# Optimization experiments

Hardware: AMD Instinct MI355X
Metric: run time of the kernel (lower is better)

The kernel has to match this reference:

```python
import jax, jax.numpy as jnp
import numpy as np

V = 16384      # total nodes
G = 32         # nodes per graph (512 graphs)
D = 256        # node embedding dim == hidden_size
N = 8          # heads
H = 32         # head size
I = 1024       # intermediate size
LN_EPS = 1e-12


def _layer_norm(x, g, b):
    mu = jnp.mean(x, axis=-1, keepdims=True)
    var = jnp.mean(jnp.square(x - mu), axis=-1, keepdims=True)
    return (x - mu) * jax.lax.rsqrt(var + LN_EPS) * g + b


def setup_inputs() -> dict:
    key = jax.random.key(0)
    ks = jax.random.split(key, 5)
    node_embeddings = jax.random.normal(ks[0], (V, D), jnp.float32)
    # fully-connected pairs within each graph of size G (sorted by source node)
    idx = np.arange(V, dtype=np.int32).reshape(-1, G)          # [num_graphs, G]
    src = np.repeat(idx, G, axis=1).reshape(-1)                # [P]
    dst = np.tile(idx, (1, G)).reshape(-1)                     # [P]
    in_graph_node_pairs = jnp.asarray(np.stack([src, dst], axis=-1))  # [P, 2]
    s = 0.02
    return {
        "node_embeddings": node_embeddings,
        "in_graph_node_pairs": in_graph_node_pairs,
        "W_qkv": jax.random.normal(ks[1], (D, 3 * N * H), jnp.float32) * s,
        "W_o": jax.random.normal(ks[2], (N * H, D), jnp.float32) * s,
        "ln1_g": jnp.ones((D,), jnp.float32),
        "ln1_b": jnp.zeros((D,), jnp.float32),
        "W_i": jax.random.normal(ks[3], (D, I), jnp.float32) * s,
        "W_out2": jax.random.normal(ks[4], (I, D), jnp.float32) * s,
        "ln2_g": jnp.ones((D,), jnp.float32),
        "ln2_b": jnp.zeros((D,), jnp.float32),
    }


def reference(node_embeddings, in_graph_node_pairs, W_qkv, W_o, ln1_g, ln1_b,
              W_i, W_out2, ln2_g, ln2_b):
    nV = node_embeddings.shape[0]
    src = in_graph_node_pairs[:, 0]
    dst = in_graph_node_pairs[:, 1]
    # QKV projection -> [V, N, 3H] -> split
    qkv = (node_embeddings @ W_qkv).reshape(nV, N, 3 * H)
    q, k, v = jnp.split(qkv, 3, axis=-1)                       # each [V, N, H]
    # per-pair scores [P, N]
    scores = jnp.einsum('phi,phi->ph', q[src], k[dst]) / jnp.sqrt(jnp.float32(H))
    # segment softmax over source node, all heads at once
    m = jax.ops.segment_max(scores, src, num_segments=nV)       # [V, N]
    e = jnp.exp(scores - m[src])
    denom = jax.ops.segment_sum(e, src, num_segments=nV)        # [V, N]
    w = e / denom[src]                                          # [P, N]
    # weighted value scatter-sum -> [V, N, H]
    wv = w[:, :, None] * v[dst]
    att = jax.ops.segment_sum(wv, src, num_segments=nV).reshape(nV, N * H)
    # output projection + residual + LN
    pre = _layer_norm(att @ W_o + node_embeddings, ln1_g, ln1_b)
    inter = jax.nn.gelu(pre @ W_i, approximate=False)
    out = _layer_norm(inter @ W_out2 + pre, ln2_g, ln2_b)
    return out
```

## Files before the change

kernel.cpp:

```cpp
#include <hip/hip_runtime.h>
#include <math.h>

#define V 16384
#define D 256
#define NH 256
#define THREE_NH 768
#define IDIM 1024
#define LN_EPS 1e-12f

typedef short s16x8 __attribute__((ext_vector_type(8)));
typedef float f32x4 __attribute__((ext_vector_type(4)));

__device__ inline unsigned short f2bf(float f) {
    unsigned u = __float_as_uint(f);
    u += 0x7fffu + ((u >> 16) & 1u);
    return (unsigned short)(u >> 16);
}
__device__ inline float bf2f(unsigned short s) {
    return __uint_as_float(((unsigned)s) << 16);
}
__device__ inline float bflo(unsigned v) { return __uint_as_float(v << 16); }
__device__ inline float bfhi(unsigned v) { return __uint_as_float(v & 0xffff0000u); }

__device__ inline void gl2lds16(const unsigned short* g, unsigned short* l) {
    __builtin_amdgcn_global_load_lds(
        (__attribute__((address_space(1))) void*)(g),
        (__attribute__((address_space(3))) void*)(l), 16, 0, 0);
}

template <int ROWS_T>
__device__ inline void stage(const unsigned short* __restrict__ src, size_t row0,
                             int ldk, int k0, unsigned short* lds, int wv, int lane) {
    constexpr int PER_WAVE = ROWS_T / 32;
    #pragma unroll
    for (int i = 0; i < PER_WAVE; ++i) {
        const int seg = wv * PER_WAVE + i;
        const int r = seg * 8 + (lane >> 3);
        const int c = (lane & 7) ^ (r & 7);
        gl2lds16(src + (row0 + (size_t)r) * ldk + k0 + c * 8, lds + seg * 512);
    }
}

__device__ inline s16x8 fragld(const unsigned short* lds, int row, int chunk) {
    return *(const s16x8*)&lds[row * 64 + ((chunk ^ (row & 7)) << 3)];
}

__global__ __launch_bounds__(256) void prep(const float* __restrict__ X,
                                            unsigned short* __restrict__ Xb,
                                            const float* __restrict__ Wqkv,
                                            const float* __restrict__ Wo,
                                            const float* __restrict__ Wi,
                                            const float* __restrict__ Wo2,
                                            unsigned short* __restrict__ WqkvT,
                                            unsigned short* __restrict__ WoT,
                                            unsigned short* __restrict__ WiT,
                                            unsigned short* __restrict__ Wo2T) {
    const int b = blockIdx.x, t = threadIdx.x;
    if (b >= 768) {
        int i = (b - 768) * 256 + t;
        float4 v = ((const float4*)X)[i];
        ushort4 o;
        o.x = f2bf(v.x); o.y = f2bf(v.y); o.z = f2bf(v.z); o.w = f2bf(v.w);
        ((ushort4*)Xb)[i] = o;
        return;
    }
    __shared__ float tile[32][33];
    const float* W; unsigned short* Wt; int K, N, bx, by;
    if (b < 192)      { W = Wqkv; Wt = WqkvT; K = 256;  N = 768;  bx = b & 7;          by = b >> 3; }
    else if (b < 256) { W = Wo;   Wt = WoT;   K = 256;  N = 256;  bx = (b - 192) & 7;  by = (b - 192) >> 3; }
    else if (b < 512) { W = Wi;   Wt = WiT;   K = 256;  N = 1024; bx = (b - 256) & 7;  by = (b - 256) >> 3; }
    else              { W = Wo2;  Wt = Wo2T;  K = 1024; N = 256;  bx = (b - 512) & 31; by = (b - 512) >> 5; }
    const int k0 = bx * 32, n0 = by * 32;
    #pragma unroll
    for (int p = 0; p < 4; ++p) {
        int idx = t + p * 256, r = idx >> 5, c = idx & 31;
        tile[r][c] = W[(size_t)(k0 + r) * N + n0 + c];
    }
    __syncthreads();
    #pragma unroll
    for (int p = 0; p < 4; ++p) {
        int idx = t + p * 256, r = idx >> 5, c = idx & 31;
        Wt[(size_t)(n0 + r) * K + k0 + c] = f2bf(tile[c][r]);
    }
}

template <int K, int N, int EPI>
__global__ __launch_bounds__(256) void gemm128(const unsigned short* __restrict__ A,
                                               const unsigned short* __restrict__ Bt,
                                               unsigned short* __restrict__ C) {
    __shared__ unsigned short As[128 * 64];
    __shared__ unsigned short Bs[128 * 64];
    const int t = threadIdx.x;
    const int r0 = blockIdx.x * 128, c0 = blockIdx.y * 128;
    const int wv = t >> 6, lane = t & 63, q = lane >> 4, l16 = lane & 15;
    const int wr = (wv >> 1) * 64, wc = (wv & 1) * 64;
    f32x4 acc[4][4] = {};

    for (int k0 = 0; k0 < K; k0 += 64) {
        __syncthreads();
        stage<128>(A,  (size_t)r0, K, k0, As, wv, lane);
        stage<128>(Bt, (size_t)c0, K, k0, Bs, wv, lane);
        __builtin_amdgcn_s_waitcnt(0);
        __syncthreads();
        #pragma unroll
        for (int kk2 = 0; kk2 < 2; ++kk2) {
            s16x8 af[4], bfr[4];
            #pragma unroll
            for (int mf = 0; mf < 4; ++mf)
                af[mf] = fragld(As, wr + mf * 16 + l16, kk2 * 4 + q);
            #pragma unroll
            for (int nf = 0; nf < 4; ++nf)
                bfr[nf] = fragld(Bs, wc + nf * 16 + l16, kk2 * 4 + q);
            #pragma unroll
            for (int mf = 0; mf < 4; ++mf)
                #pragma unroll
                for (int nf = 0; nf < 4; ++nf)
                    acc[mf][nf] = __builtin_amdgcn_mfma_f32_16x16x32_bf16(af[mf], bfr[nf], acc[mf][nf], 0, 0, 0);
        }
    }

    #pragma unroll
    for (int mf = 0; mf < 4; ++mf)
        #pragma unroll
        for (int nf = 0; nf < 4; ++nf) {
            const int cg = c0 + wc + nf * 16 + l16;
            #pragma unroll
            for (int r = 0; r < 4; ++r) {
                const int rg = r0 + wr + mf * 16 + q * 4 + r;
                float v = acc[mf][nf][r];
                if (EPI == 1) v = 0.5f * v * (1.f + erff(v * 0.70710678118654752f));
                C[(size_t)rg * N + cg] = f2bf(v);
            }
        }
}

template <int K, bool OUTF, bool RESBF>
__global__ __launch_bounds__(256) void gemm_ln(const unsigned short* __restrict__ A,
                                               const unsigned short* __restrict__ Bt,
                                               const void* __restrict__ resv,
                                               const float* __restrict__ gamma,
                                               const float* __restrict__ beta,
                                               float* __restrict__ outf,
                                               unsigned short* __restrict__ outb) {
    __shared__ unsigned short As[32 * 64];
    __shared__ unsigned short Bs[256 * 64];
    __shared__ float2 partial[4][32];
    __shared__ float2 stats[32];
    const int t = threadIdx.x, r0 = blockIdx.x * 32;
    const int wv = t >> 6, lane = t & 63, q = lane >> 4, l16 = lane & 15;
    const int wc = wv * 64;
    f32x4 acc[2][4] = {};

    for (int k0 = 0; k0 < K; k0 += 64) {
        __syncthreads();
        stage<32>(A, (size_t)r0, K, k0, As, wv, lane);
        stage<256>(Bt, 0, K, k0, Bs, wv, lane);
        __builtin_amdgcn_s_waitcnt(0);
        __syncthreads();
        #pragma unroll
        for (int kk2 = 0; kk2 < 2; ++kk2) {
            s16x8 af[2], bfr[4];
            #pragma unroll
            for (int mf = 0; mf < 2; ++mf)
                af[mf] = fragld(As, mf * 16 + l16, kk2 * 4 + q);
            #pragma unroll
            for (int nf = 0; nf < 4; ++nf)
                bfr[nf] = fragld(Bs, wc + nf * 16 + l16, kk2 * 4 + q);
            #pragma unroll
            for (int mf = 0; mf < 2; ++mf)
                #pragma unroll
                for (int nf = 0; nf < 4; ++nf)
                    acc[mf][nf] = __builtin_amdgcn_mfma_f32_16x16x32_bf16(af[mf], bfr[nf], acc[mf][nf], 0, 0, 0);
        }
    }

    #pragma unroll
    for (int mf = 0; mf < 2; ++mf)
        #pragma unroll
        for (int nf = 0; nf < 4; ++nf) {
            const int cg = wc + nf * 16 + l16;
            #pragma unroll
            for (int r = 0; r < 4; ++r) {
                const size_t idx = (size_t)(r0 + mf * 16 + q * 4 + r) * NH + cg;
                float rv;
                if (RESBF) rv = bf2f(((const unsigned short*)resv)[idx]);
                else       rv = ((const float*)resv)[idx];
                acc[mf][nf][r] += rv;
            }
        }

    #pragma unroll
    for (int mf = 0; mf < 2; ++mf) {
        float s[4] = {0.f, 0.f, 0.f, 0.f}, ss[4] = {0.f, 0.f, 0.f, 0.f};
        #pragma unroll
        for (int nf = 0; nf < 4; ++nf)
            #pragma unroll
            for (int r = 0; r < 4; ++r) {
                float v = acc[mf][nf][r];
                s[r] += v; ss[r] += v * v;
            }
        #pragma unroll
        for (int off = 1; off < 16; off <<= 1)
            #pragma unroll
            for (int r = 0; r < 4; ++r) {
                s[r]  += __shfl_xor(s[r],  off);
                ss[r] += __shfl_xor(ss[r], off);
            }
        if (l16 == 0)
            #pragma unroll
            for (int r = 0; r < 4; ++r)
                partial[wv][mf * 16 + q * 4 + r] = make_float2(s[r], ss[r]);
    }
    __syncthreads();
    if (t < 32) {
        float s = 0.f, ss = 0.f;
        #pragma unroll
        for (int w = 0; w < 4; ++w) { s += partial[w][t].x; ss += partial[w][t].y; }
        float mu  = s * (1.f / 256.f);
        float var = ss * (1.f / 256.f) - mu * mu;
        stats[t] = make_float2(mu, rsqrtf(var + LN_EPS));
    }
    __syncthreads();

    #pragma unroll
    for (int mf = 0; mf < 2; ++mf)
        #pragma unroll
        for (int nf = 0; nf < 4; ++nf) {
            const int cg = wc + nf * 16 + l16;
            const float g = gamma[cg], b = beta[cg];
            #pragma unroll
            for (int r = 0; r < 4; ++r) {
                const int rl = mf * 16 + q * 4 + r;
                const float2 st = stats[rl];
                float v = (acc[mf][nf][r] - st.x) * st.y * g + b;
                const size_t idx = (size_t)(r0 + rl) * NH + cg;
                if (OUTF) outf[idx] = v;
                else      outb[idx] = f2bf(v);
            }
        }
}

#define LDR 776
__global__ __launch_bounds__(256) void attln(const unsigned short* __restrict__ qkv,
                                             const unsigned short* __restrict__ WoT,
                                             const float* __restrict__ X,
                                             const float* __restrict__ gamma,
                                             const float* __restrict__ beta,
                                             unsigned short* __restrict__ preb) {
    __shared__ unsigned short smem[33536 + 320];
    unsigned short* s  = smem;
    unsigned short* pt = smem + 24832;
    unsigned short* at = smem;
    unsigned short* Bs = smem + 8192;
    float2* partial = (float2*)(smem + 24832);
    float2* stats   = (float2*)(smem + 24832 + 512);

    const int g = blockIdx.x;
    const int t = threadIdx.x;
    const int h = t >> 5, u = t & 31;
    const int ub = u & 7;
    const int us = u >> 3;
    const int qc = h * 96;

    const unsigned short* src = qkv + (size_t)g * 32 * THREE_NH;
    #pragma unroll
    for (int pp = 0; pp < 12; ++pp) {
        int c = t + pp * 256;
        int row = c / 96, col8 = c % 96;
        s16x8 vv = *(const s16x8*)&src[c * 8];
        *(s16x8*)&s[row * LDR + col8 * 8] = vv;
    }
    __syncthreads();

    float sc[4][8];
    #pragma unroll
    for (int di = 0; di < 4; ++di)
        #pragma unroll
        for (int dj = 0; dj < 8; ++dj) sc[di][dj] = 0.f;

    for (int kq = 0; kq < 8; ++kq) {
        float qv[4][4];
        #pragma unroll
        for (int di = 0; di < 4; ++di) {
            uint2 v = *(const uint2*)&s[(ub + 8 * di) * LDR + qc + 4 * kq];
            qv[di][0] = bflo(v.x); qv[di][1] = bfhi(v.x);
            qv[di][2] = bflo(v.y); qv[di][3] = bfhi(v.y);
        }
        #pragma unroll
        for (int dj = 0; dj < 8; ++dj) {
            uint2 v = *(const uint2*)&s[(us + 4 * dj) * LDR + qc + 32 + 4 * kq];
            float kv[4];
            kv[0] = bflo(v.x); kv[1] = bfhi(v.x);
            kv[2] = bflo(v.y); kv[3] = bfhi(v.y);
            #pragma unroll
            for (int di = 0; di < 4; ++di)
                #pragma unroll
                for (int kk = 0; kk < 4; ++kk)
                    sc[di][dj] = fmaf(qv[di][kk], kv[kk], sc[di][dj]);
        }
    }

    #pragma unroll
    for (int di = 0; di < 4; ++di) {
        float m = sc[di][0];
        #pragma unroll
        for (int dj = 1; dj < 8; ++dj) m = fmaxf(m, sc[di][dj]);
        m = fmaxf(m, __shfl_xor(m, 8));
        m = fmaxf(m, __shfl_xor(m, 16));
        float sum = 0.f;
        #pragma unroll
        for (int dj = 0; dj < 8; ++dj) {
            float e = __expf((sc[di][dj] - m) * 0.17677669529663687f);
            sc[di][dj] = e;
            sum += e;
        }
        sum += __shfl_xor(sum, 8);
        sum += __shfl_xor(sum, 16);
        float inv = 1.f / sum;
        const int rb = h * 1088 + (ub + 8 * di) * 34;
        #pragma unroll
        for (int dj = 0; dj < 8; ++dj)
            pt[rb + us + 4 * dj] = f2bf(sc[di][dj] * inv);
    }
    __syncthreads();

    const int vc = qc + 64, d0 = us * 8;
    float o[4][8];
    #pragma unroll
    for (int di = 0; di < 4; ++di)
        #pragma unroll
        for (int dd = 0; dd < 8; ++dd) o[di][dd] = 0.f;

    for (int j = 0; j < 32; ++j) {
        float pv[4];
        #pragma unroll
        for (int di = 0; di < 4; ++di)
            pv[di] = bf2f(pt[h * 1088 + (ub + 8 * di) * 34 + j]);
        #pragma unroll
        for (int dq = 0; dq < 2; ++dq) {
            uint2 v = *(const uint2*)&s[j * LDR + vc + d0 + 4 * dq];
            float v0 = bflo(v.x), v1 = bfhi(v.x), v2 = bflo(v.y), v3 = bfhi(v.y);
            #pragma unroll
            for (int di = 0; di < 4; ++di) {
                o[di][dq * 4 + 0] = fmaf(pv[di], v0, o[di][dq * 4 + 0]);
                o[di][dq * 4 + 1] = fmaf(pv[di], v1, o[di][dq * 4 + 1]);
                o[di][dq * 4 + 2] = fmaf(pv[di], v2, o[di][dq * 4 + 2]);
                o[di][dq * 4 + 3] = fmaf(pv[di], v3, o[di][dq * 4 + 3]);
            }
        }
    }
    __syncthreads();

    {
        const int col = h * 32 + d0;
        const int kb = col >> 6, c = (col & 63) >> 3;
        #pragma unroll
        for (int di = 0; di < 4; ++di) {
            const int i = ub + 8 * di;
            s16x8 ov;
            #pragma unroll
            for (int dd = 0; dd < 8; ++dd) ov[dd] = (short)f2bf(o[di][dd]);
            *(s16x8*)&at[kb * 2048 + i * 64 + ((c ^ (i & 7)) << 3)] = ov;
        }
    }

    const int wv = t >> 6, lane = t & 63, q = lane >> 4, l16 = lane & 15;
    const int wc = wv * 64;
    const int r0 = g * 32;
    f32x4 acc[2][4] = {};

    for (int k0 = 0; k0 < 256; k0 += 64) {
        __syncthreads();
        stage<256>(WoT, 0, 256, k0, Bs, wv, lane);
        __builtin_amdgcn_s_waitcnt(0);
        __syncthreads();
        const unsigned short* atk = at + (k0 >> 6) * 2048;
        #pragma unroll
        for (int kk2 = 0; kk2 < 2; ++kk2) {
            s16x8 af[2], bfr[4];
            #pragma unroll
            for (int mf = 0; mf < 2; ++mf)
                af[mf] = fragld(atk, mf * 16 + l16, kk2 * 4 + q);
            #pragma unroll
            for (int nf = 0; nf < 4; ++nf)
                bfr[nf] = fragld(Bs, wc + nf * 16 + l16, kk2 * 4 + q);
            #pragma unroll
            for (int mf = 0; mf < 2; ++mf)
                #pragma unroll
                for (int nf = 0; nf < 4; ++nf)
                    acc[mf][nf] = __builtin_amdgcn_mfma_f32_16x16x32_bf16(af[mf], bfr[nf], acc[mf][nf], 0, 0, 0);
        }
    }

    #pragma unroll
    for (int mf = 0; mf < 2; ++mf)
        #pragma unroll
        for (int nf = 0; nf < 4; ++nf) {
            const int cg = wc + nf * 16 + l16;
            #pragma unroll
            for (int r = 0; r < 4; ++r)
                acc[mf][nf][r] += X[(size_t)(r0 + mf * 16 + q * 4 + r) * NH + cg];
        }

    #pragma unroll
    for (int mf = 0; mf < 2; ++mf) {
        float sp[4] = {0.f, 0.f, 0.f, 0.f}, ssp[4] = {0.f, 0.f, 0.f, 0.f};
        #pragma unroll
        for (int nf = 0; nf < 4; ++nf)
            #pragma unroll
            for (int r = 0; r < 4; ++r) {
                float v = acc[mf][nf][r];
                sp[r] += v; ssp[r] += v * v;
            }
        #pragma unroll
        for (int off = 1; off < 16; off <<= 1)
            #pragma unroll
            for (int r = 0; r < 4; ++r) {
                sp[r]  += __shfl_xor(sp[r],  off);
                ssp[r] += __shfl_xor(ssp[r], off);
            }
        if (l16 == 0)
            #pragma unroll
            for (int r = 0; r < 4; ++r)
                partial[wv * 32 + mf * 16 + q * 4 + r] = make_float2(sp[r], ssp[r]);
    }
    __syncthreads();
    if (t < 32) {
        float sv = 0.f, ssv = 0.f;
        #pragma unroll
        for (int w = 0; w < 4; ++w) { sv += partial[w * 32 + t].x; ssv += partial[w * 32 + t].y; }
        float mu  = sv * (1.f / 256.f);
        float var = ssv * (1.f / 256.f) - mu * mu;
        stats[t] = make_float2(mu, rsqrtf(var + LN_EPS));
    }
    __syncthreads();

    #pragma unroll
    for (int mf = 0; mf < 2; ++mf)
        #pragma unroll
        for (int nf = 0; nf < 4; ++nf) {
            const int cg = wc + nf * 16 + l16;
            const float gm = gamma[cg], bt = beta[cg];
            #pragma unroll
            for (int r = 0; r < 4; ++r) {
                const int rl = mf * 16 + q * 4 + r;
                const float2 st = stats[rl];
                float v = (acc[mf][nf][r] - st.x) * st.y * gm + bt;
                preb[(size_t)(r0 + rl) * NH + cg] = f2bf(v);
            }
        }
}

extern "C" void kernel_launch(void* const* d_in, const int* in_sizes, int n_in,
                              void* d_out, int out_size, void* d_ws, size_t ws_size,
                              hipStream_t stream) {
    const float* X      = (const float*)d_in[0];
    const float* W_qkv  = (const float*)d_in[2];
    const float* W_o    = (const float*)d_in[3];
    const float* ln1_g  = (const float*)d_in[4];
    const float* ln1_b  = (const float*)d_in[5];
    const float* W_i    = (const float*)d_in[6];
    const float* W_out2 = (const float*)d_in[7];
    const float* ln2_g  = (const float*)d_in[8];
    const float* ln2_b  = (const float*)d_in[9];
    float* out = (float*)d_out;

    char* ws = (char*)d_ws;
    unsigned short* Xbf   = (unsigned short*)(ws);
    unsigned short* qkvb  = (unsigned short*)(ws + 8388608);
    unsigned short* preb  = (unsigned short*)(ws + 58720256);
    unsigned short* WqkvT = (unsigned short*)(ws + 67108864);
    unsigned short* WoT   = (unsigned short*)(ws + 67502080);
    unsigned short* WiT   = (unsigned short*)(ws + 67633152);
    unsigned short* Wo2T  = (unsigned short*)(ws + 68157440);
    unsigned short* interb = (unsigned short*)(ws);

    dim3 blk(256);
    hipLaunchKernelGGL(prep, dim3(768 + V * D / 4 / 256), blk, 0, stream,
                       X, Xbf, W_qkv, W_o, W_i, W_out2, WqkvT, WoT, WiT, Wo2T);

    hipLaunchKernelGGL((gemm128<D, THREE_NH, 0>), dim3(V / 128, THREE_NH / 128), blk, 0, stream,
                       Xbf, WqkvT, qkvb);
    hipLaunchKernelGGL(attln, dim3(V / 32), blk, 0, stream,
                       qkvb, WoT, X, ln1_g, ln1_b, preb);
    hipLaunchKernelGGL((gemm128<D, IDIM, 1>), dim3(V / 128, IDIM / 128), blk, 0, stream,
                       preb, WiT, interb);
    hipLaunchKernelGGL((gemm_ln<IDIM, true, true>), dim3(V / 32), blk, 0, stream,
                       interb, Wo2T, (const void*)preb, ln2_g, ln2_b, out, (unsigned short*)nullptr);
}
```

Before: 164.8 us.

## Fuse all five kernels into one persistent kernel with grid barriers

```diff
diff --git a/kernel.cpp b/kernel.cpp
--- a/kernel.cpp
+++ b/kernel.cpp
@@ -45,53 +45,30 @@
     return *(const s16x8*)&lds[row * 64 + ((chunk ^ (row & 7)) << 3)];
 }
 
-__global__ __launch_bounds__(256) void prep(const float* __restrict__ X,
-                                            unsigned short* __restrict__ Xb,
-                                            const float* __restrict__ Wqkv,
-                                            const float* __restrict__ Wo,
-                                            const float* __restrict__ Wi,
-                                            const float* __restrict__ Wo2,
-                                            unsigned short* __restrict__ WqkvT,
-                                            unsigned short* __restrict__ WoT,
-                                            unsigned short* __restrict__ WiT,
-                                            unsigned short* __restrict__ Wo2T) {
-    const int b = blockIdx.x, t = threadIdx.x;
-    if (b >= 768) {
-        int i = (b - 768) * 256 + t;
-        float4 v = ((const float4*)X)[i];
-        ushort4 o;
-        o.x = f2bf(v.x); o.y = f2bf(v.y); o.z = f2bf(v.z); o.w = f2bf(v.w);
-        ((ushort4*)Xb)[i] = o;
-        return;
-    }
-    __shared__ float tile[32][33];
-    const float* W; unsigned short* Wt; int K, N, bx, by;
-    if (b < 192)      { W = Wqkv; Wt = WqkvT; K = 256;  N = 768;  bx = b & 7;          by = b >> 3; }
-    else if (b < 256) { W = Wo;   Wt = WoT;   K = 256;  N = 256;  bx = (b - 192) & 7;  by = (b - 192) >> 3; }
-    else if (b < 512) { W = Wi;   Wt = WiT;   K = 256;  N = 1024; bx = (b - 256) & 7;  by = (b - 256) >> 3; }
-    else              { W = Wo2;  Wt = Wo2T;  K = 1024; N = 256;  bx = (b - 512) & 31; by = (b - 512) >> 5; }
-    const int k0 = bx * 32, n0 = by * 32;
-    #pragma unroll
-    for (int p = 0; p < 4; ++p) {
-        int idx = t + p * 256, r = idx >> 5, c = idx & 31;
-        tile[r][c] = W[(size_t)(k0 + r) * N + n0 + c];
-    }
+__device__ inline void gridbar(unsigned* ctr) {
     __syncthreads();
-    #pragma unroll
-    for (int p = 0; p < 4; ++p) {
-        int idx = t + p * 256, r = idx >> 5, c = idx & 31;
-        Wt[(size_t)(n0 + r) * K + k0 + c] = f2bf(tile[c][r]);
-    }
+    if (threadIdx.x == 0) {
+        __hip_atomic_fetch_add(ctr, 1u, __ATOMIC_RELEASE, __HIP_MEMORY_SCOPE_AGENT);
+        for (unsigned i = 0; i < (1u << 20); ++i) {
+            if (__hip_atomic_load(ctr, __ATOMIC_ACQUIRE, __HIP_MEMORY_SCOPE_AGENT) >= 512u)
+                break;
+            __builtin_amdgcn_s_sleep(8);
+        }
+        __threadfence();
+    }
+    __syncthreads();
+}
+
+__global__ __launch_bounds__(128) void initctr(unsigned* __restrict__ ctr) {
+    ctr[threadIdx.x] = 0u;
 }
 
 template <int K, int N, int EPI>
-__global__ __launch_bounds__(256) void gemm128(const unsigned short* __restrict__ A,
-                                               const unsigned short* __restrict__ Bt,
-                                               unsigned short* __restrict__ C) {
-    __shared__ unsigned short As[128 * 64];
-    __shared__ unsigned short Bs[128 * 64];
-    const int t = threadIdx.x;
-    const int r0 = blockIdx.x * 128, c0 = blockIdx.y * 128;
+__device__ inline void gemm_tile(const unsigned short* __restrict__ A,
+                                 const unsigned short* __restrict__ Bt,
+                                 unsigned short* __restrict__ C,
+                                 int r0, int c0, unsigned short* As,
+                                 unsigned short* Bs, int t) {
     const int wv = t >> 6, lane = t & 63, q = lane >> 4, l16 = lane & 15;
     const int wr = (wv >> 1) * 64, wc = (wv & 1) * 64;
     f32x4 acc[4][4] = {};
@@ -118,6 +95,7 @@
                     acc[mf][nf] = __builtin_amdgcn_mfma_f32_16x16x32_bf16(af[mf], bfr[nf], acc[mf][nf], 0, 0, 0);
         }
     }
+    __syncthreads();
 
     #pragma unroll
     for (int mf = 0; mf < 4; ++mf)
@@ -134,321 +112,374 @@
         }
 }
 
-template <int K, bool OUTF, bool RESBF>
-__global__ __launch_bounds__(256) void gemm_ln(const unsigned short* __restrict__ A,
-                                               const unsigned short* __restrict__ Bt,
-                                               const void* __restrict__ resv,
-                                               const float* __restrict__ gamma,
-                                               const float* __restrict__ beta,
-                                               float* __restrict__ outf,
-                                               unsigned short* __restrict__ outb) {
-    __shared__ unsigned short As[32 * 64];
-    __shared__ unsigned short Bs[256 * 64];
-    __shared__ float2 partial[4][32];
-    __shared__ float2 stats[32];
-    const int t = threadIdx.x, r0 = blockIdx.x * 32;
-    const int wv = t >> 6, lane = t & 63, q = lane >> 4, l16 = lane & 15;
-    const int wc = wv * 64;
-    f32x4 acc[2][4] = {};
-
-    for (int k0 = 0; k0 < K; k0 += 64) {
-        __syncthreads();
-        stage<32>(A, (size_t)r0, K, k0, As, wv, lane);
-        stage<256>(Bt, 0, K, k0, Bs, wv, lane);
-        __builtin_amdgcn_s_waitcnt(0);
-        __syncthreads();
-        #pragma unroll
-        for (int kk2 = 0; kk2 < 2; ++kk2) {
-            s16x8 af[2], bfr[4];
-            #pragma unroll
-            for (int mf = 0; mf < 2; ++mf)
-                af[mf] = fragld(As, mf * 16 + l16, kk2 * 4 + q);
+#define LDR 776
+__global__ __launch_bounds__(256, 2) void mega(const float* __restrict__ X,
+                                               const float* __restrict__ Wqkv,
+                                               const float* __restrict__ Wo,
+                                               const float* __restrict__ Wi,
+                                               const float* __restrict__ Wo2,
+                                               const float* __restrict__ ln1g,
+                                               const float* __restrict__ ln1b,
+                                               const float* __restrict__ ln2g,
+                                               const float* __restrict__ ln2b,
+                                               float* __restrict__ out,
+                                               char* __restrict__ ws,
+                                               unsigned* __restrict__ ctr) {
+    __shared__ unsigned long long smem8[8464];
+    unsigned short* smem = (unsigned short*)smem8;
+
+    unsigned short* Xbf    = (unsigned short*)(ws);
+    unsigned short* qkvb   = (unsigned short*)(ws + 8388608);
+    unsigned short* preb   = (unsigned short*)(ws + 58720256);
+    unsigned short* WqkvT  = (unsigned short*)(ws + 67108864);
+    unsigned short* WoT    = (unsigned short*)(ws + 67502080);
+    unsigned short* WiT    = (unsigned short*)(ws + 67633152);
+    unsigned short* Wo2T   = (unsigned short*)(ws + 68157440);
+    unsigned short* interb = (unsigned short*)(ws);
+
+    const int t = threadIdx.x;
+
+    for (int b = blockIdx.x; b < 4864; b += 512) {
+        if (b >= 768) {
+            int i = (b - 768) * 256 + t;
+            float4 v = ((const float4*)X)[i];
+            ushort4 o;
+            o.x = f2bf(v.x); o.y = f2bf(v.y); o.z = f2bf(v.z); o.w = f2bf(v.w);
+            ((ushort4*)Xbf)[i] = o;
+        } else {
+            float* tile = (float*)smem;
+            const float* W; unsigned short* Wt; int K, N, bx, by;
+            if (b < 192)      { W = Wqkv; Wt = WqkvT; K = 256;  N = 768;  bx = b & 7;          by = b >> 3; }
+            else if (b < 256) { W = Wo;   Wt = WoT;   K = 256;  N = 256;  bx = (b - 192) & 7;  by = (b - 192) >> 3; }
+            else if (b < 512) { W = Wi;   Wt = WiT;   K = 256;  N = 1024; bx = (b - 256) & 7;  by = (b - 256) >> 3; }
+            else              { W = Wo2;  Wt = Wo2T;  K = 1024; N = 256;  bx = (b - 512) & 31; by = (b - 512) >> 5; }
+            const int k0 = bx * 32, n0 = by * 32;
+            __syncthreads();
+            #pragma unroll
+            for (int p = 0; p < 4; ++p) {
+                int idx = t + p * 256, r = idx >> 5, c = idx & 31;
+                tile[r * 33 + c] = W[(size_t)(k0 + r) * N + n0 + c];
+            }
+            __syncthreads();
+            #pragma unroll
+            for (int p = 0; p < 4; ++p) {
+                int idx = t + p * 256, r = idx >> 5, c = idx & 31;
+                Wt[(size_t)(n0 + r) * K + k0 + c] = f2bf(tile[c * 33 + r]);
+            }
+        }
+    }
+    gridbar(ctr);
+
+    for (int u = blockIdx.x; u < 768; u += 512) {
+        const int rb = u / 6, cb = u % 6;
+        gemm_tile<D, THREE_NH, 0>(Xbf, WqkvT, qkvb, rb * 128, cb * 128,
+                                  smem, smem + 8192, t);
+    }
+    gridbar(ctr + 32);
+
+    {
+        unsigned short* s  = smem;
+        unsigned short* pt = smem + 24832;
+        unsigned short* at = smem;
+        unsigned short* Bs = smem + 8192;
+        float2* partial = (float2*)(smem + 24832);
+        float2* stats   = (float2*)(smem + 24832 + 512);
+
+        const int g = blockIdx.x;
+        const int h = t >> 5, u = t & 31;
+        const int ub = u & 7;
+        const int us = u >> 3;
+        const int qc = h * 96;
+
+        const unsigned short* src = qkvb + (size_t)g * 32 * THREE_NH;
+        #pragma unroll
+        for (int pp = 0; pp < 12; ++pp) {
+            int c = t + pp * 256;
+            int row = c / 96, col8 = c % 96;
+            s16x8 vv = *(const s16x8*)&src[c * 8];
+            *(s16x8*)&s[row * LDR + col8 * 8] = vv;
+        }
+        __syncthreads();
+
+        float sc[4][8];
+        #pragma unroll
+        for (int di = 0; di < 4; ++di)
+            #pragma unroll
+            for (int dj = 0; dj < 8; ++dj) sc[di][dj] = 0.f;
+
+        for (int kq = 0; kq < 8; ++kq) {
+            float qv[4][4];
+            #pragma unroll
+            for (int di = 0; di < 4; ++di) {
+                uint2 v = *(const uint2*)&s[(ub + 8 * di) * LDR + qc + 4 * kq];
+                qv[di][0] = bflo(v.x); qv[di][1] = bfhi(v.x);
+                qv[di][2] = bflo(v.y); qv[di][3] = bfhi(v.y);
+            }
+            #pragma unroll
+            for (int dj = 0; dj < 8; ++dj) {
+                uint2 v = *(const uint2*)&s[(us + 4 * dj) * LDR + qc + 32 + 4 * kq];
+                float kv[4];
+                kv[0] = bflo(v.x); kv[1] = bfhi(v.x);
+                kv[2] = bflo(v.y); kv[3] = bfhi(v.y);
+                #pragma unroll
+                for (int di = 0; di < 4; ++di)
+                    #pragma unroll
+                    for (int kk = 0; kk < 4; ++kk)
+                        sc[di][dj] = fmaf(qv[di][kk], kv[kk], sc[di][dj]);
+            }
+        }
+
+        #pragma unroll
+        for (int di = 0; di < 4; ++di) {
+            float m = sc[di][0];
+            #pragma unroll
+            for (int dj = 1; dj < 8; ++dj) m = fmaxf(m, sc[di][dj]);
+            m = fmaxf(m, __shfl_xor(m, 8));
+            m = fmaxf(m, __shfl_xor(m, 16));
+            float sum = 0.f;
+            #pragma unroll
+            for (int dj = 0; dj < 8; ++dj) {
+                float e = __expf((sc[di][dj] - m) * 0.17677669529663687f);
+                sc[di][dj] = e;
+                sum += e;
+            }
+            sum += __shfl_xor(sum, 8);
+            sum += __shfl_xor(sum, 16);
+            float inv = 1.f / sum;
+            const int rb = h * 1088 + (ub + 8 * di) * 34;
+            #pragma unroll
+            for (int dj = 0; dj < 8; ++dj)
+                pt[rb + us + 4 * dj] = f2bf(sc[di][dj] * inv);
+        }
+        __syncthreads();
+
+        const int vc = qc + 64, d0 = us * 8;
+        float o[4][8];
+        #pragma unroll
+        for (int di = 0; di < 4; ++di)
+            #pragma unroll
+            for (int dd = 0; dd < 8; ++dd) o[di][dd] = 0.f;
+
+        for (int j = 0; j < 32; ++j) {
+            float pv[4];
+            #pragma unroll
+            for (int di = 0; di < 4; ++di)
+                pv[di] = bf2f(pt[h * 1088 + (ub + 8 * di) * 34 + j]);
+            #pragma unroll
+            for (int dq = 0; dq < 2; ++dq) {
+                uint2 v = *(const uint2*)&s[j * LDR + vc + d0 + 4 * dq];
+                float v0 = bflo(v.x), v1 = bfhi(v.x), v2 = bflo(v.y), v3 = bfhi(v.y);
+                #pragma unroll
+                for (int di = 0; di < 4; ++di) {
+                    o[di][dq * 4 + 0] = fmaf(pv[di], v0, o[di][dq * 4 + 0]);
+                    o[di][dq * 4 + 1] = fmaf(pv[di], v1, o[di][dq * 4 + 1]);
+                    o[di][dq * 4 + 2] = fmaf(pv[di], v2, o[di][dq * 4 + 2]);
+                    o[di][dq * 4 + 3] = fmaf(pv[di], v3, o[di][dq * 4 + 3]);
+                }
+            }
+        }
+        __syncthreads();
+
+        {
+            const int col = h * 32 + d0;
+            const int kb = col >> 6, c = (col & 63) >> 3;
+            #pragma unroll
+            for (int di = 0; di < 4; ++di) {
+                const int i = ub + 8 * di;
+                s16x8 ov;
+                #pragma unroll
+                for (int dd = 0; dd < 8; ++dd) ov[dd] = (short)f2bf(o[di][dd]);
+                *(s16x8*)&at[kb * 2048 + i * 64 + ((c ^ (i & 7)) << 3)] = ov;
+            }
+        }
+
+        const int wv = t >> 6, lane = t & 63, q = lane >> 4, l16 = lane & 15;
+        const int wc = wv * 64;
+        const int r0 = g * 32;
+        f32x4 acc[2][4] = {};
+
+        for (int k0 = 0; k0 < 256; k0 += 64) {
+            __syncthreads();
+            stage<256>(WoT, 0, 256, k0, Bs, wv, lane);
+            __builtin_amdgcn_s_waitcnt(0);
+            __syncthreads();
+            const unsigned short* atk = at + (k0 >> 6) * 2048;
+            #pragma unroll
+            for (int kk2 = 0; kk2 < 2; ++kk2) {
+                s16x8 af[2], bfr[4];
+                #pragma unroll
+                for (int mf = 0; mf < 2; ++mf)
+                    af[mf] = fragld(atk, mf * 16 + l16, kk2 * 4 + q);
+                #pragma unroll
+                for (int nf = 0; nf < 4; ++nf)
+                    bfr[nf] = fragld(Bs, wc + nf * 16 + l16, kk2 * 4 + q);
+                #pragma unroll
+                for (int mf = 0; mf < 2; ++mf)
+                    #pragma unroll
+                    for (int nf = 0; nf < 4; ++nf)
+                        acc[mf][nf] = __builtin_amdgcn_mfma_f32_16x16x32_bf16(af[mf], bfr[nf], acc[mf][nf], 0, 0, 0);
+            }
+        }
+
+        #pragma unroll
+        for (int mf = 0; mf < 2; ++mf)
+            #pragma unroll
+            for (int nf = 0; nf < 4; ++nf) {
+                const int cg = wc + nf * 16 + l16;
+                #pragma unroll
+                for (int r = 0; r < 4; ++r)
+                    acc[mf][nf][r] += X[(size_t)(r0 + mf * 16 + q * 4 + r) * NH + cg];
+            }
+
+        #pragma unroll
+        for (int mf = 0; mf < 2; ++mf) {
+            float sp[4] = {0.f, 0.f, 0.f, 0.f}, ssp[4] = {0.f, 0.f, 0.f, 0.f};
             #pragma unroll
             for (int nf = 0; nf < 4; ++nf)
-                bfr[nf] = fragld(Bs, wc + nf * 16 + l16, kk2 * 4 + q);
-            #pragma unroll
-            for (int mf = 0; mf < 2; ++mf)
+                #pragma unroll
+                for (int r = 0; r < 4; ++r) {
+                    float v = acc[mf][nf][r];
+                    sp[r] += v; ssp[r] += v * v;
+                }
+            #pragma unroll
+            for (int off = 1; off < 16; off <<= 1)
+                #pragma unroll
+                for (int r = 0; r < 4; ++r) {
+                    sp[r]  += __shfl_xor(sp[r],  off);
+                    ssp[r] += __shfl_xor(ssp[r], off);
+                }
+            if (l16 == 0)
+                #pragma unroll
+                for (int r = 0; r < 4; ++r)
+                    partial[wv * 32 + mf * 16 + q * 4 + r] = make_float2(sp[r], ssp[r]);
+        }
+        __syncthreads();
+        if (t < 32) {
+            float sv = 0.f, ssv = 0.f;
+            #pragma unroll
+            for (int w = 0; w < 4; ++w) { sv += partial[w * 32 + t].x; ssv += partial[w * 32 + t].y; }
+            float mu  = sv * (1.f / 256.f);
+            float var = ssv * (1.f / 256.f) - mu * mu;
+            stats[t] = make_float2(mu, rsqrtf(var + LN_EPS));
+        }
+        __syncthreads();
+
+        #pragma unroll
+        for (int mf = 0; mf < 2; ++mf)
+            #pragma unroll
+            for (int nf = 0; nf < 4; ++nf) {
+                const int cg = wc + nf * 16 + l16;
+                const float gm = ln1g[cg], bt = ln1b[cg];
+                #pragma unroll
+                for (int r = 0; r < 4; ++r) {
+                    const int rl = mf * 16 + q * 4 + r;
+                    const float2 st = stats[rl];
+                    float v = (acc[mf][nf][r] - st.x) * st.y * gm + bt;
+                    preb[(size_t)(r0 + rl) * NH + cg] = f2bf(v);
+                }
+            }
+    }
+    gridbar(ctr + 64);
+
+    for (int u = blockIdx.x; u < 1024; u += 512) {
+        const int rb = u >> 3, cb = u & 7;
+        gemm_tile<D, IDIM, 1>(preb, WiT, interb, rb * 128, cb * 128,
+                              smem, smem + 8192, t);
+    }
+    gridbar(ctr + 96);
+
+    {
+        unsigned short* As = smem;
+        unsigned short* Bs = smem + 2048;
+        float2* partial = (float2*)(smem + 18432);
+        float2* stats   = (float2*)(smem + 18944);
+        const int r0 = blockIdx.x * 32;
+        const int wv = t >> 6, lane = t & 63, q = lane >> 4, l16 = lane & 15;
+        const int wc = wv * 64;
+        f32x4 acc[2][4] = {};
+
+        for (int k0 = 0; k0 < IDIM; k0 += 64) {
+            __syncthreads();
+            stage<32>(interb, (size_t)r0, IDIM, k0, As, wv, lane);
+            stage<256>(Wo2T, 0, IDIM, k0, Bs, wv, lane);
+            __builtin_amdgcn_s_waitcnt(0);
+            __syncthreads();
+            #pragma unroll
+            for (int kk2 = 0; kk2 < 2; ++kk2) {
+                s16x8 af[2], bfr[4];
+                #pragma unroll
+                for (int mf = 0; mf < 2; ++mf)
+                    af[mf] = fragld(As, mf * 16 + l16, kk2 * 4 + q);
                 #pragma unroll
                 for (int nf = 0; nf < 4; ++nf)
-                    acc[mf][nf] = __builtin_amdgcn_mfma_f32_16x16x32_bf16(af[mf], bfr[nf], acc[mf][nf], 0, 0, 0);
-        }
-    }
-
-    #pragma unroll
-    for (int mf = 0; mf < 2; ++mf)
-        #pragma unroll
-        for (int nf = 0; nf < 4; ++nf) {
-            const int cg = wc + nf * 16 + l16;
-            #pragma unroll
-            for (int r = 0; r < 4; ++r) {
-                const size_t idx = (size_t)(r0 + mf * 16 + q * 4 + r) * NH + cg;
-                float rv;
-                if (RESBF) rv = bf2f(((const unsigned short*)resv)[idx]);
-                else       rv = ((const float*)resv)[idx];
-                acc[mf][nf][r] += rv;
-            }
-        }
-
-    #pragma unroll
-    for (int mf = 0; mf < 2; ++mf) {
-        float s[4] = {0.f, 0.f, 0.f, 0.f}, ss[4] = {0.f, 0.f, 0.f, 0.f};
-        #pragma unroll
-        for (int nf = 0; nf < 4; ++nf)
-            #pragma unroll
-            for (int r = 0; r < 4; ++r) {
-                float v = acc[mf][nf][r];
-                s[r] += v; ss[r] += v * v;
-            }
-        #pragma unroll
-        for (int off = 1; off < 16; off <<= 1)
-            #pragma unroll
-            for (int r = 0; r < 4; ++r) {
-                s[r]  += __shfl_xor(s[r],  off);
-                ss[r] += __shfl_xor(ss[r], off);
-            }
-        if (l16 == 0)
-            #pragma unroll
-            for (int r = 0; r < 4; ++r)
-                partial[wv][mf * 16 + q * 4 + r] = make_float2(s[r], ss[r]);
-    }
-    __syncthreads();
-    if (t < 32) {
-        float s = 0.f, ss = 0.f;
-        #pragma unroll
-        for (int w = 0; w < 4; ++w) { s += partial[w][t].x; ss += partial[w][t].y; }
-        float mu  = s * (1.f / 256.f);
-        float var = ss * (1.f / 256.f) - mu * mu;
-        stats[t] = make_float2(mu, rsqrtf(var + LN_EPS));
-    }
-    __syncthreads();
-
-    #pragma unroll
-    for (int mf = 0; mf < 2; ++mf)
-        #pragma unroll
-        for (int nf = 0; nf < 4; ++nf) {
-            const int cg = wc + nf * 16 + l16;
-            const float g = gamma[cg], b = beta[cg];
-            #pragma unroll
-            for (int r = 0; r < 4; ++r) {
-                const int rl = mf * 16 + q * 4 + r;
-                const float2 st = stats[rl];
-                float v = (acc[mf][nf][r] - st.x) * st.y * g + b;
-                const size_t idx = (size_t)(r0 + rl) * NH + cg;
-                if (OUTF) outf[idx] = v;
-                else      outb[idx] = f2bf(v);
-            }
-        }
-}
-
-#define LDR 776
-__global__ __launch_bounds__(256) void attln(const unsigned short* __restrict__ qkv,
-                                             const unsigned short* __restrict__ WoT,
-                                             const float* __restrict__ X,
-                                             const float* __restrict__ gamma,
-                                             const float* __restrict__ beta,
-                                             unsigned short* __restrict__ preb) {
-    __shared__ unsigned short smem[33536 + 320];
-    unsigned short* s  = smem;
-    unsigned short* pt = smem + 24832;
-    unsigned short* at = smem;
-    unsigned short* Bs = smem + 8192;
-    float2* partial = (float2*)(smem + 24832);
-    float2* stats   = (float2*)(smem + 24832 + 512);
-
-    const int g = blockIdx.x;
-    const int t = threadIdx.x;
-    const int h = t >> 5, u = t & 31;
-    const int ub = u & 7;
-    const int us = u >> 3;
-    const int qc = h * 96;
-
-    const unsigned short* src = qkv + (size_t)g * 32 * THREE_NH;
-    #pragma unroll
-    for (int pp = 0; pp < 12; ++pp) {
-        int c = t + pp * 256;
-        int row = c / 96, col8 = c % 96;
-        s16x8 vv = *(const s16x8*)&src[c * 8];
-        *(s16x8*)&s[row * LDR + col8 * 8] = vv;
-    }
-    __syncthreads();
-
-    float sc[4][8];
-    #pragma unroll
-    for (int di = 0; di < 4; ++di)
-        #pragma unroll
-        for (int dj = 0; dj < 8; ++dj) sc[di][dj] = 0.f;
-
-    for (int kq = 0; kq < 8; ++kq) {
-        float qv[4][4];
-        #pragma unroll
-        for (int di = 0; di < 4; ++di) {
-            uint2 v = *(const uint2*)&s[(ub + 8 * di) * LDR + qc + 4 * kq];
-            qv[di][0] = bflo(v.x); qv[di][1] = bfhi(v.x);
-            qv[di][2] = bflo(v.y); qv[di][3] = bfhi(v.y);
-        }
-        #pragma unroll
-        for (int dj = 0; dj < 8; ++dj) {
-            uint2 v = *(const uint2*)&s[(us + 4 * dj) * LDR + qc + 32 + 4 * kq];
-            float kv[4];
-            kv[0] = bflo(v.x); kv[1] = bfhi(v.x);
-            kv[2] = bflo(v.y); kv[3] = bfhi(v.y);
-            #pragma unroll
-            for (int di = 0; di < 4; ++di)
-                #pragma unroll
-                for (int kk = 0; kk < 4; ++kk)
-                    sc[di][dj] = fmaf(qv[di][kk], kv[kk], sc[di][dj]);
-        }
-    }
-
-    #pragma unroll
-    for (int di = 0; di < 4; ++di) {
-        float m = sc[di][0];
-        #pragma unroll
-        for (int dj = 1; dj < 8; ++dj) m = fmaxf(m, sc[di][dj]);
-        m = fmaxf(m, __shfl_xor(m, 8));
-        m = fmaxf(m, __shfl_xor(m, 16));
-        float sum = 0.f;
-        #pragma unroll
-        for (int dj = 0; dj < 8; ++dj) {
-            float e = __expf((sc[di][dj] - m) * 0.17677669529663687f);
-            sc[di][dj] = e;
-            sum += e;
-        }
-        sum += __shfl_xor(sum, 8);
-        sum += __shfl_xor(sum, 16);
-        float inv = 1.f / sum;
-        const int rb = h * 1088 + (ub + 8 * di) * 34;
-        #pragma unroll
-        for (int dj = 0; dj < 8; ++dj)
-            pt[rb + us + 4 * dj] = f2bf(sc[di][dj] * inv);
-    }
-    __syncthreads();
-
-    const int vc = qc + 64, d0 = us * 8;
-    float o[4][8];
-    #pragma unroll
-    for (int di = 0; di < 4; ++di)
-        #pragma unroll
-        for (int dd = 0; dd < 8; ++dd) o[di][dd] = 0.f;
-
-    for (int j = 0; j < 32; ++j) {
-        float pv[4];
-        #pragma unroll
-        for (int di = 0; di < 4; ++di)
-            pv[di] = bf2f(pt[h * 1088 + (ub + 8 * di) * 34 + j]);
-        #pragma unroll
-        for (int dq = 0; dq < 2; ++dq) {
-            uint2 v = *(const uint2*)&s[j * LDR + vc + d0 + 4 * dq];
-            float v0 = bflo(v.x), v1 = bfhi(v.x), v2 = bflo(v.y), v3 = bfhi(v.y);
-            #pragma unroll
-            for (int di = 0; di < 4; ++di) {
-                o[di][dq * 4 + 0] = fmaf(pv[di], v0, o[di][dq * 4 + 0]);
-                o[di][dq * 4 + 1] = fmaf(pv[di], v1, o[di][dq * 4 + 1]);
-                o[di][dq * 4 + 2] = fmaf(pv[di], v2, o[di][dq * 4 + 2]);
-                o[di][dq * 4 + 3] = fmaf(pv[di], v3, o[di][dq * 4 + 3]);
-            }
-        }
-    }
-    __syncthreads();
-
-    {
-        const int col = h * 32 + d0;
-        const int kb = col >> 6, c = (col & 63) >> 3;
-        #pragma unroll
-        for (int di = 0; di < 4; ++di) {
-            const int i = ub + 8 * di;
-            s16x8 ov;
-            #pragma unroll
-            for (int dd = 0; dd < 8; ++dd) ov[dd] = (short)f2bf(o[di][dd]);
-            *(s16x8*)&at[kb * 2048 + i * 64 + ((c ^ (i & 7)) << 3)] = ov;
-        }
-    }
-
-    const int wv = t >> 6, lane = t & 63, q = lane >> 4, l16 = lane & 15;
-    const int wc = wv * 64;
-    const int r0 = g * 32;
-    f32x4 acc[2][4] = {};
-
-    for (int k0 = 0; k0 < 256; k0 += 64) {
-        __syncthreads();
-        stage<256>(WoT, 0, 256, k0, Bs, wv, lane);
-        __builtin_amdgcn_s_waitcnt(0);
-        __syncthreads();
-        const unsigned short* atk = at + (k0 >> 6) * 2048;
-        #pragma unroll
-        for (int kk2 = 0; kk2 < 2; ++kk2) {
-            s16x8 af[2], bfr[4];
-            #pragma unroll
-            for (int mf = 0; mf < 2; ++mf)
-                af[mf] = fragld(atk, mf * 16 + l16, kk2 * 4 + q);
+                    bfr[nf] = fragld(Bs, wc + nf * 16 + l16, kk2 * 4 + q);
+                #pragma unroll
+                for (int mf = 0; mf < 2; ++mf)
+                    #pragma unroll
+                    for (int nf = 0; nf < 4; ++nf)
+                        acc[mf][nf] = __builtin_amdgcn_mfma_f32_16x16x32_bf16(af[mf], bfr[nf], acc[mf][nf], 0, 0, 0);
+            }
+        }
+
+        #pragma unroll
+        for (int mf = 0; mf < 2; ++mf)
+            #pragma unroll
+            for (int nf = 0; nf < 4; ++nf) {
+                const int cg = wc + nf * 16 + l16;
+                #pragma unroll
+                for (int r = 0; r < 4; ++r) {
+                    const size_t idx = (size_t)(r0 + mf * 16 + q * 4 + r) * NH + cg;
+                    acc[mf][nf][r] += bf2f(preb[idx]);
+                }
+            }
+
+        #pragma unroll
+        for (int mf = 0; mf < 2; ++mf) {
+            float sp[4] = {0.f, 0.f, 0.f, 0.f}, ssp[4] = {0.f, 0.f, 0.f, 0.f};
             #pragma unroll
             for (int nf = 0; nf < 4; ++nf)
-                bfr[nf] = fragld(Bs, wc + nf * 16 + l16, kk2 * 4 + q);
-            #pragma unroll
-            for (int mf = 0; mf < 2; ++mf)
-                #pragma unroll
-                for (int nf = 0; nf < 4; ++nf)
-                    acc[mf][nf] = __builtin_amdgcn_mfma_f32_16x16x32_bf16(af[mf], bfr[nf], acc[mf][nf], 0, 0, 0);
-        }
-    }
-
-    #pragma unroll
-    for (int mf = 0; mf < 2; ++mf)
-        #pragma unroll
-        for (int nf = 0; nf < 4; ++nf) {
-            const int cg = wc + nf * 16 + l16;
-            #pragma unroll
-            for (int r = 0; r < 4; ++r)
-                acc[mf][nf][r] += X[(size_t)(r0 + mf * 16 + q * 4 + r) * NH + cg];
-        }
-
-    #pragma unroll
-    for (int mf = 0; mf < 2; ++mf) {
-        float sp[4] = {0.f, 0.f, 0.f, 0.f}, ssp[4] = {0.f, 0.f, 0.f, 0.f};
-        #pragma unroll
-        for (int nf = 0; nf < 4; ++nf)
-            #pragma unroll
-            for (int r = 0; r < 4; ++r) {
-                float v = acc[mf][nf][r];
-                sp[r] += v; ssp[r] += v * v;
-            }
-        #pragma unroll
-        for (int off = 1; off < 16; off <<= 1)
-            #pragma unroll
-            for (int r = 0; r < 4; ++r) {
-                sp[r]  += __shfl_xor(sp[r],  off);
-                ssp[r] += __shfl_xor(ssp[r], off);
-            }
-        if (l16 == 0)
-            #pragma unroll
-            for (int r = 0; r < 4; ++r)
-                partial[wv * 32 + mf * 16 + q * 4 + r] = make_float2(sp[r], ssp[r]);
-    }
-    __syncthreads();
-    if (t < 32) {
-        float sv = 0.f, ssv = 0.f;
-        #pragma unroll
-        for (int w = 0; w < 4; ++w) { sv += partial[w * 32 + t].x; ssv += partial[w * 32 + t].y; }
-        float mu  = sv * (1.f / 256.f);
-        float var = ssv * (1.f / 256.f) - mu * mu;
-        stats[t] = make_float2(mu, rsqrtf(var + LN_EPS));
-    }
-    __syncthreads();
-
-    #pragma unroll
-    for (int mf = 0; mf < 2; ++mf)
-        #pragma unroll
-        for (int nf = 0; nf < 4; ++nf) {
-            const int cg = wc + nf * 16 + l16;
-            const float gm = gamma[cg], bt = beta[cg];
-            #pragma unroll
-            for (int r = 0; r < 4; ++r) {
-                const int rl = mf * 16 + q * 4 + r;
-                const float2 st = stats[rl];
-                float v = (acc[mf][nf][r] - st.x) * st.y * gm + bt;
-                preb[(size_t)(r0 + rl) * NH + cg] = f2bf(v);
-            }
-        }
+                #pragma unroll
+                for (int r = 0; r < 4; ++r) {
+                    float v = acc[mf][nf][r];
+                    sp[r] += v; ssp[r] += v * v;
+                }
+            #pragma unroll
+            for (int off = 1; off < 16; off <<= 1)
+                #pragma unroll
+                for (int r = 0; r < 4; ++r) {
+                    sp[r]  += __shfl_xor(sp[r],  off);
+                    ssp[r] += __shfl_xor(ssp[r], off);
+                }
+            if (l16 == 0)
+                #pragma unroll
+                for (int r = 0; r < 4; ++r)
+                    partial[wv * 32 + mf * 16 + q * 4 + r] = make_float2(sp[r], ssp[r]);
+        }
+        __syncthreads();
+        if (t < 32) {
+            float sv = 0.f, ssv = 0.f;
+            #pragma unroll
+            for (int w = 0; w < 4; ++w) { sv += partial[w * 32 + t].x; ssv += partial[w * 32 + t].y; }
+            float mu  = sv * (1.f / 256.f);
+            float var = ssv * (1.f / 256.f) - mu * mu;
+            stats[t] = make_float2(mu, rsqrtf(var + LN_EPS));
+        }
+        __syncthreads();
+
+        #pragma unroll
+        for (int mf = 0; mf < 2; ++mf)
+            #pragma unroll
+            for (int nf = 0; nf < 4; ++nf) {
+                const int cg = wc + nf * 16 + l16;
+                const float gm = ln2g[cg], bt = ln2b[cg];
+                #pragma unroll
+                for (int r = 0; r < 4; ++r) {
+                    const int rl = mf * 16 + q * 4 + r;
+                    const float2 st = stats[rl];
+                    out[(size_t)(r0 + rl) * NH + cg] = (acc[mf][nf][r] - st.x) * st.y * gm + bt;
+                }
+            }
+    }
 }
 
 extern "C" void kernel_launch(void* const* d_in, const int* in_sizes, int n_in,
@@ -464,27 +495,11 @@
     const float* ln2_g  = (const float*)d_in[8];
     const float* ln2_b  = (const float*)d_in[9];
     float* out = (float*)d_out;
-
-    char* ws = (char*)d_ws;
-    unsigned short* Xbf   = (unsigned short*)(ws);
-    unsigned short* qkvb  = (unsigned short*)(ws + 8388608);
-    unsigned short* preb  = (unsigned short*)(ws + 58720256);
-    unsigned short* WqkvT = (unsigned short*)(ws + 67108864);
-    unsigned short* WoT   = (unsigned short*)(ws + 67502080);
-    unsigned short* WiT   = (unsigned short*)(ws + 67633152);
-    unsigned short* Wo2T  = (unsigned short*)(ws + 68157440);
-    unsigned short* interb = (unsigned short*)(ws);
-
-    dim3 blk(256);
-    hipLaunchKernelGGL(prep, dim3(768 + V * D / 4 / 256), blk, 0, stream,
-                       X, Xbf, W_qkv, W_o, W_i, W_out2, WqkvT, WoT, WiT, Wo2T);
-
-    hipLaunchKernelGGL((gemm128<D, THREE_NH, 0>), dim3(V / 128, THREE_NH / 128), blk, 0, stream,
-                       Xbf, WqkvT, qkvb);
-    hipLaunchKernelGGL(attln, dim3(V / 32), blk, 0, stream,
-                       qkvb, WoT, X, ln1_g, ln1_b, preb);
-    hipLaunchKernelGGL((gemm128<D, IDIM, 1>), dim3(V / 128, IDIM / 128), blk, 0, stream,
-                       preb, WiT, interb);
-    hipLaunchKernelGGL((gemm_ln<IDIM, true, true>), dim3(V / 32), blk, 0, stream,
-                       interb, Wo2T, (const void*)preb, ln2_g, ln2_b, out, (unsigned short*)nullptr);
-}
+    char* ws   = (char*)d_ws;
+    unsigned* ctr = (unsigned*)(ws + 41943040);
+
+    hipLaunchKernelGGL(initctr, dim3(1), dim3(128), 0, stream, ctr);
+    hipLaunchKernelGGL(mega, dim3(512), dim3(256), 0, stream,
+                       X, W_qkv, W_o, W_i, W_out2, ln1_g, ln1_b,
+                       ln2_g, ln2_b, out, ws, ctr);
+}
```

Result: slower. 463.5 us (+181.3%).
